# Kernel optimization log

Measured on AMD Instinct MI355X. Metric: run time of the kernel, lower is better.

## Reference

```python
import jax, jax.numpy as jnp
import numpy as np

DELTA_VAR = 0.5
DELTA_DIST = 1.5
ALPHA = 1.0
BETA = 1.0
C = 4096        # number of superpixels (static for segment_sum)
NE = 16384      # number of RAG edges


def setup_inputs() -> dict:
    key = jax.random.key(0)
    k1, k2, k3, k4 = jax.random.split(key, 4)
    embeddings = jax.random.normal(k1, (1, 16, 1024, 1024), dtype=jnp.float32)
    sp_seg = jax.random.randint(k2, (1, 1, 1024, 1024), 0, C)
    edges = jax.random.randint(k3, (2, NE), 0, C)
    weights = jax.random.uniform(k4, (NE,), dtype=jnp.float32)
    return {"embeddings": embeddings, "weights": weights, "sp_seg": sp_seg, "edges": edges}


def reference(embeddings, weights, sp_seg, edges):
    # embeddings: (1,E,H,W); sp_seg: (1,1,H,W) int labels in [0,C)
    E = embeddings.shape[1]
    emb = embeddings.reshape(E, -1).T          # (P,E) pixel-major
    seg = sp_seg.reshape(-1)                   # (P,)
    counts = jax.ops.segment_sum(jnp.ones(seg.shape, emb.dtype), seg, num_segments=C)  # (C,)
    sums = jax.ops.segment_sum(emb, seg, num_segments=C)                               # (C,E)
    n = jnp.maximum(counts, 1.0)               # guard empty segments (orig would div-by-0)
    means = sums / n[:, None]                  # (C,E) superpixel mean embeddings
    # intra-superpixel: d = 1 - <mean_c, emb_p> at pixels of segment c, hinge at delta_var,
    # normalized per-pixel by segment size, then averaged over C
    d_intra = 1.0 - jnp.sum(means[seg] * emb, axis=-1)            # (P,)
    intra = jnp.sum(jnp.maximum(d_intra - DELTA_VAR, 0.0) / n[seg]) / C
    # inter-superpixel: gather edge endpoint means, weighted hinge at delta_dist
    u, v = edges[0], edges[1]
    d_inter = 1.0 - jnp.sum(means[u] * means[v], axis=-1)         # (Ne,)
    inter = jnp.sum(jnp.maximum(DELTA_DIST - d_inter * weights, 0.0)) / edges.shape[1]
    return ALPHA * inter + BETA * intra
```

## Files before the change

kernel.cpp:

```cpp
#include <hip/hip_runtime.h>

#define C_SEG 4096
#define E_CH 16
#define NE_EDGES 16384
#define P_PIX (1024 * 1024)
#define NCHUNK 32
#define CHUNK_PIX (P_PIX / NCHUNK)
#define SCALE 262144.0f
#define INV_SCALE (1.0f / 262144.0f)


__global__ __launch_bounds__(512) void kA(const float* __restrict__ emb,
                                          const int* __restrict__ seg,
                                          float* __restrict__ sums_part,
                                          float* __restrict__ cnt_part) {
    __shared__ int bins[C_SEG];
    const int chunk = blockIdx.x;
    const int g = blockIdx.y;
    const int t = threadIdx.x;
    const int base = chunk * CHUNK_PIX;

    for (int i = t; i < C_SEG; i += 512) bins[i] = 0;
    __syncthreads();

    if (g == 16) {
        for (int it = 0; it < 16; ++it) {
            const int idx = base + (it * 512 + t) * 4;
            const int4 s4 = *(const int4*)(seg + idx);
            atomicAdd(&bins[s4.x], 1);
            atomicAdd(&bins[s4.y], 1);
            atomicAdd(&bins[s4.z], 1);
            atomicAdd(&bins[s4.w], 1);
        }
        __syncthreads();
        float* cd = cnt_part + (size_t)chunk * C_SEG;
        for (int i = t; i < C_SEG; i += 512) cd[i] = (float)bins[i];
    } else {
        const float* ec = emb + (size_t)g * P_PIX;
        for (int it = 0; it < 16; ++it) {
            const int idx = base + (it * 512 + t) * 4;
            const int4 s4 = *(const int4*)(seg + idx);
            const float4 v = *(const float4*)(ec + idx);
            atomicAdd(&bins[s4.x], __float2int_rn(v.x * SCALE));
            atomicAdd(&bins[s4.y], __float2int_rn(v.y * SCALE));
            atomicAdd(&bins[s4.z], __float2int_rn(v.z * SCALE));
            atomicAdd(&bins[s4.w], __float2int_rn(v.w * SCALE));
        }
        __syncthreads();
        float* dst = sums_part + ((size_t)g * NCHUNK + chunk) * C_SEG;
        for (int i = t; i < C_SEG; i += 512)
            dst[i] = (float)bins[i] * INV_SCALE;
    }
}

__global__ __launch_bounds__(256) void kB(const float* __restrict__ sums_part,
                                          const float* __restrict__ cnt_part,
                                          float* __restrict__ msum,
                                          float* __restrict__ inv_n) {
    const int vb = blockIdx.x, t = threadIdx.x;
    if (vb < 256) {
        const int c = vb >> 4;
        const int s = (vb & 15) * 256 + t;
        const float* src = sums_part + (size_t)c * NCHUNK * C_SEG + s;
        float acc = 0.0f;
#pragma unroll
        for (int k = 0; k < NCHUNK; ++k) acc += src[(size_t)k * C_SEG];
        msum[s * E_CH + c] = acc;
    } else {
        const int s = (vb - 256) * 256 + t;
        float acc = 0.0f;
#pragma unroll
        for (int k = 0; k < NCHUNK; ++k) acc += cnt_part[(size_t)k * C_SEG + s];
        inv_n[s] = 1.0f / fmaxf(acc, 1.0f);
    }
}

__global__ __launch_bounds__(256) void kC(const float* __restrict__ emb,
                                          const int* __restrict__ seg,
                                          const int* __restrict__ edges,
                                          const float* __restrict__ w,
                                          const float* __restrict__ msum,
                                          const float* __restrict__ inv_n,
                                          float* __restrict__ part) {
    const int b = blockIdx.x, t = threadIdx.x;
    const int q = b * 256 + t;
    const int4 s4 = *(const int4*)(seg + q * 4);

    float mA[16], mB[16], mC[16], mD[16];
#pragma unroll
    for (int j = 0; j < 4; ++j) {
        ((float4*)mA)[j] = ((const float4*)(msum + s4.x * E_CH))[j];
        ((float4*)mB)[j] = ((const float4*)(msum + s4.y * E_CH))[j];
        ((float4*)mC)[j] = ((const float4*)(msum + s4.z * E_CH))[j];
        ((float4*)mD)[j] = ((const float4*)(msum + s4.w * E_CH))[j];
    }
    const float inx = inv_n[s4.x], iny = inv_n[s4.y];
    const float inz = inv_n[s4.z], inw = inv_n[s4.w];

    const float4* emb4 = (const float4*)emb;
    float4 e[16];
#pragma unroll
    for (int c = 0; c < 16; ++c) e[c] = emb4[(size_t)c * (P_PIX / 4) + q];

    float dx = 0.f, dy = 0.f, dz = 0.f, dw = 0.f;
#pragma unroll
    for (int c = 0; c < 16; ++c) {
        dx = fmaf(e[c].x, mA[c], dx);
        dy = fmaf(e[c].y, mB[c], dy);
        dz = fmaf(e[c].z, mC[c], dz);
        dw = fmaf(e[c].w, mD[c], dw);
    }

    float v = (fmaxf(0.5f - inx * dx, 0.0f) * inx +
               fmaxf(0.5f - iny * dy, 0.0f) * iny +
               fmaxf(0.5f - inz * dz, 0.0f) * inz +
               fmaxf(0.5f - inw * dw, 0.0f) * inw) *
              (1.0f / (float)C_SEG);

    if (t < 16) {
        const int e2 = b * 16 + t;
        const int u = edges[e2];
        const int vv = edges[NE_EDGES + e2];
        const float4* mu = (const float4*)(msum + u * E_CH);
        const float4* mv = (const float4*)(msum + vv * E_CH);
        float dot = 0.0f;
#pragma unroll
        for (int j = 0; j < 4; ++j) {
            const float4 a = mu[j];
            const float4 bb = mv[j];
            dot = fmaf(a.x, bb.x, dot);
            dot = fmaf(a.y, bb.y, dot);
            dot = fmaf(a.z, bb.z, dot);
            dot = fmaf(a.w, bb.w, dot);
        }
        const float d = 1.0f - inv_n[u] * inv_n[vv] * dot;
        v += fmaxf(1.5f - d * w[e2], 0.0f) * (1.0f / (float)NE_EDGES);
    }

    for (int o = 32; o > 0; o >>= 1) v += __shfl_down(v, o, 64);
    __shared__ float red[4];
    if ((t & 63) == 0) red[t >> 6] = v;
    __syncthreads();
    if (t == 0) part[b] = red[0] + red[1] + red[2] + red[3];
}

__global__ __launch_bounds__(256) void kF(const float* __restrict__ part,
                                          float* __restrict__ out) {
    float v = 0.0f;
    for (int i = threadIdx.x; i < 1024; i += 256) v += part[i];
    for (int o = 32; o > 0; o >>= 1) v += __shfl_down(v, o, 64);
    __shared__ float red[4];
    const int t = threadIdx.x;
    if ((t & 63) == 0) red[t >> 6] = v;
    __syncthreads();
    if (t == 0) out[0] = red[0] + red[1] + red[2] + red[3];
}

extern "C" void kernel_launch(void* const* d_in, const int* in_sizes, int n_in,
                              void* d_out, int out_size, void* d_ws,
                              size_t ws_size, hipStream_t stream) {
    const float* emb = (const float*)d_in[0];
    const float* weights = (const float*)d_in[1];
    const int* seg = (const int*)d_in[2];
    const int* edges = (const int*)d_in[3];
    float* out = (float*)d_out;

    char* ws = (char*)d_ws;
    float* sums_part = (float*)(ws);
    float* cnt_part = (float*)(ws + 0x800000);
    float* msum = (float*)(ws + 0x880000);
    float* invn = (float*)(ws + 0x8C0000);
    float* part = (float*)(ws + 0x8C4000);

    dim3 gA(NCHUNK, 17);
    kA<<<gA, 512, 0, stream>>>(emb, seg, sums_part, cnt_part);
    kB<<<272, 256, 0, stream>>>(sums_part, cnt_part, msum, invn);
    kC<<<1024, 256, 0, stream>>>(emb, seg, edges, weights, msum, invn, part);
    kF<<<1, 256, 0, stream>>>(part, out);
}
```

Baseline: 134.5 us.

## Pack two channel sums into 64-bit shared atomics and store normalized means

The segment-sum kernel now packs two biased fixed-point channel values into a single 64-bit shared-memory atomic. This halves the number of atomic operations and the number of blocks that re-read the segment labels. The reduction kernel sums raw integers exactly, removes the bias, and writes normalized means, so the loss kernel no longer multiplies by the inverse count. The loss kernel also goes from four pixels per thread to two, with twice as many blocks, to cut register pressure. The bias makes 32-bit lane overflow possible if per-chunk sums grow large, and 64-bit LDS atomics may be slower per operation.

Measured after the change: 142.4 us. +5.9%, slower.

```diff
diff --git a/kernel.cpp b/kernel.cpp
--- a/kernel.cpp
+++ b/kernel.cpp
@@ -8,121 +8,134 @@
 #define CHUNK_PIX (P_PIX / NCHUNK)
 #define SCALE 262144.0f
 #define INV_SCALE (1.0f / 262144.0f)
+#define BIAS 4194304
 
 
 __global__ __launch_bounds__(512) void kA(const float* __restrict__ emb,
                                           const int* __restrict__ seg,
-                                          float* __restrict__ sums_part,
-                                          float* __restrict__ cnt_part) {
-    __shared__ int bins[C_SEG];
+                                          int* __restrict__ sums_raw,
+                                          int* __restrict__ cnt_raw) {
+    __shared__ unsigned long long bins[C_SEG];
     const int chunk = blockIdx.x;
     const int g = blockIdx.y;
     const int t = threadIdx.x;
     const int base = chunk * CHUNK_PIX;
 
-    for (int i = t; i < C_SEG; i += 512) bins[i] = 0;
-    __syncthreads();
-
-    if (g == 16) {
+    if (g == 8) {
+        int* ib = (int*)bins;
+        for (int i = t; i < C_SEG; i += 512) ib[i] = 0;
+        __syncthreads();
         for (int it = 0; it < 16; ++it) {
             const int idx = base + (it * 512 + t) * 4;
             const int4 s4 = *(const int4*)(seg + idx);
-            atomicAdd(&bins[s4.x], 1);
-            atomicAdd(&bins[s4.y], 1);
-            atomicAdd(&bins[s4.z], 1);
-            atomicAdd(&bins[s4.w], 1);
+            atomicAdd(&ib[s4.x], 1);
+            atomicAdd(&ib[s4.y], 1);
+            atomicAdd(&ib[s4.z], 1);
+            atomicAdd(&ib[s4.w], 1);
         }
         __syncthreads();
-        float* cd = cnt_part + (size_t)chunk * C_SEG;
-        for (int i = t; i < C_SEG; i += 512) cd[i] = (float)bins[i];
+        int* cd = cnt_raw + (size_t)chunk * C_SEG;
+        for (int i = t; i < C_SEG; i += 512) cd[i] = ib[i];
     } else {
-        const float* ec = emb + (size_t)g * P_PIX;
+        for (int i = t; i < C_SEG; i += 512) bins[i] = 0ull;
+        __syncthreads();
+        const float* ea = emb + (size_t)(2 * g) * P_PIX;
+        const float* eb = emb + (size_t)(2 * g + 1) * P_PIX;
         for (int it = 0; it < 16; ++it) {
             const int idx = base + (it * 512 + t) * 4;
             const int4 s4 = *(const int4*)(seg + idx);
-            const float4 v = *(const float4*)(ec + idx);
-            atomicAdd(&bins[s4.x], __float2int_rn(v.x * SCALE));
-            atomicAdd(&bins[s4.y], __float2int_rn(v.y * SCALE));
-            atomicAdd(&bins[s4.z], __float2int_rn(v.z * SCALE));
-            atomicAdd(&bins[s4.w], __float2int_rn(v.w * SCALE));
+            const float4 va = *(const float4*)(ea + idx);
+            const float4 vb = *(const float4*)(eb + idx);
+            const unsigned long long p0 =
+                ((unsigned long long)(unsigned)(__float2int_rn(vb.x * SCALE) + BIAS) << 32) |
+                (unsigned)(__float2int_rn(va.x * SCALE) + BIAS);
+            const unsigned long long p1 =
+                ((unsigned long long)(unsigned)(__float2int_rn(vb.y * SCALE) + BIAS) << 32) |
+                (unsigned)(__float2int_rn(va.y * SCALE) + BIAS);
+            const unsigned long long p2 =
+                ((unsigned long long)(unsigned)(__float2int_rn(vb.z * SCALE) + BIAS) << 32) |
+                (unsigned)(__float2int_rn(va.z * SCALE) + BIAS);
+            const unsigned long long p3 =
+                ((unsigned long long)(unsigned)(__float2int_rn(vb.w * SCALE) + BIAS) << 32) |
+                (unsigned)(__float2int_rn(va.w * SCALE) + BIAS);
+            atomicAdd(&bins[s4.x], p0);
+            atomicAdd(&bins[s4.y], p1);
+            atomicAdd(&bins[s4.z], p2);
+            atomicAdd(&bins[s4.w], p3);
         }
         __syncthreads();
-        float* dst = sums_part + ((size_t)g * NCHUNK + chunk) * C_SEG;
-        for (int i = t; i < C_SEG; i += 512)
-            dst[i] = (float)bins[i] * INV_SCALE;
+        int* da = sums_raw + ((size_t)(2 * g) * NCHUNK + chunk) * C_SEG;
+        int* db = sums_raw + ((size_t)(2 * g + 1) * NCHUNK + chunk) * C_SEG;
+        for (int i = t; i < C_SEG; i += 512) {
+            const unsigned long long v = bins[i];
+            da[i] = (int)(unsigned)(v & 0xffffffffull);
+            db[i] = (int)(unsigned)(v >> 32);
+        }
     }
 }
 
-__global__ __launch_bounds__(256) void kB(const float* __restrict__ sums_part,
-                                          const float* __restrict__ cnt_part,
-                                          float* __restrict__ msum,
+__global__ __launch_bounds__(256) void kB(const int* __restrict__ sums_raw,
+                                          const int* __restrict__ cnt_raw,
+                                          float* __restrict__ mean,
                                           float* __restrict__ inv_n) {
     const int vb = blockIdx.x, t = threadIdx.x;
-    if (vb < 256) {
-        const int c = vb >> 4;
-        const int s = (vb & 15) * 256 + t;
-        const float* src = sums_part + (size_t)c * NCHUNK * C_SEG + s;
-        float acc = 0.0f;
+    const int c = vb >> 4;
+    const int s = (vb & 15) * 256 + t;
+    const int* src = sums_raw + (size_t)c * NCHUNK * C_SEG + s;
+    long long acc = 0;
+    int cnt = 0;
 #pragma unroll
-        for (int k = 0; k < NCHUNK; ++k) acc += src[(size_t)k * C_SEG];
-        msum[s * E_CH + c] = acc;
-    } else {
-        const int s = (vb - 256) * 256 + t;
-        float acc = 0.0f;
-#pragma unroll
-        for (int k = 0; k < NCHUNK; ++k) acc += cnt_part[(size_t)k * C_SEG + s];
-        inv_n[s] = 1.0f / fmaxf(acc, 1.0f);
+    for (int k = 0; k < NCHUNK; ++k) {
+        acc += src[(size_t)k * C_SEG];
+        cnt += cnt_raw[(size_t)k * C_SEG + s];
     }
+    acc -= (long long)cnt * (long long)BIAS;
+    const float invn = 1.0f / fmaxf((float)cnt, 1.0f);
+    mean[s * E_CH + c] = (float)acc * INV_SCALE * invn;
+    if (c == 0) inv_n[s] = invn;
 }
 
 __global__ __launch_bounds__(256) void kC(const float* __restrict__ emb,
                                           const int* __restrict__ seg,
                                           const int* __restrict__ edges,
                                           const float* __restrict__ w,
-                                          const float* __restrict__ msum,
+                                          const float* __restrict__ mean,
                                           const float* __restrict__ inv_n,
                                           float* __restrict__ part) {
     const int b = blockIdx.x, t = threadIdx.x;
     const int q = b * 256 + t;
-    const int4 s4 = *(const int4*)(seg + q * 4);
+    const int2 s2 = *(const int2*)(seg + q * 2);
 
-    float mA[16], mB[16], mC[16], mD[16];
+    float mA[16], mB[16];
 #pragma unroll
     for (int j = 0; j < 4; ++j) {
-        ((float4*)mA)[j] = ((const float4*)(msum + s4.x * E_CH))[j];
-        ((float4*)mB)[j] = ((const float4*)(msum + s4.y * E_CH))[j];
-        ((float4*)mC)[j] = ((const float4*)(msum + s4.z * E_CH))[j];
-        ((float4*)mD)[j] = ((const float4*)(msum + s4.w * E_CH))[j];
+        ((float4*)mA)[j] = ((const float4*)(mean + s2.x * E_CH))[j];
+        ((float4*)mB)[j] = ((const float4*)(mean + s2.y * E_CH))[j];
     }
-    const float inx = inv_n[s4.x], iny = inv_n[s4.y];
-    const float inz = inv_n[s4.z], inw = inv_n[s4.w];
+    const float inx = inv_n[s2.x], iny = inv_n[s2.y];
 
-    const float4* emb4 = (const float4*)emb;
-    float4 e[16];
+    const float2* emb2 = (const float2*)emb;
+    float2 e[16];
 #pragma unroll
-    for (int c = 0; c < 16; ++c) e[c] = emb4[(size_t)c * (P_PIX / 4) + q];
+    for (int c = 0; c < 16; ++c) e[c] = emb2[(size_t)c * (P_PIX / 2) + q];
 
-    float dx = 0.f, dy = 0.f, dz = 0.f, dw = 0.f;
+    float dx = 0.f, dy = 0.f;
 #pragma unroll
     for (int c = 0; c < 16; ++c) {
         dx = fmaf(e[c].x, mA[c], dx);
         dy = fmaf(e[c].y, mB[c], dy);
-        dz = fmaf(e[c].z, mC[c], dz);
-        dw = fmaf(e[c].w, mD[c], dw);
     }
 
-    float v = (fmaxf(0.5f - inx * dx, 0.0f) * inx +
-               fmaxf(0.5f - iny * dy, 0.0f) * iny +
-               fmaxf(0.5f - inz * dz, 0.0f) * inz +
-               fmaxf(0.5f - inw * dw, 0.0f) * inw) *
+    float v = (fmaxf(0.5f - dx, 0.0f) * inx +
+               fmaxf(0.5f - dy, 0.0f) * iny) *
               (1.0f / (float)C_SEG);
 
-    if (t < 16) {
-        const int e2 = b * 16 + t;
+    if (t < 8) {
+        const int e2 = b * 8 + t;
         const int u = edges[e2];
         const int vv = edges[NE_EDGES + e2];
-        const float4* mu = (const float4*)(msum + u * E_CH);
-        const float4* mv = (const float4*)(msum + vv * E_CH);
+        const float4* mu = (const float4*)(mean + u * E_CH);
+        const float4* mv = (const float4*)(mean + vv * E_CH);
         float dot = 0.0f;
 #pragma unroll
         for (int j = 0; j < 4; ++j) {
@@ -133,7 +146,7 @@
             dot = fmaf(a.z, bb.z, dot);
             dot = fmaf(a.w, bb.w, dot);
         }
-        const float d = 1.0f - inv_n[u] * inv_n[vv] * dot;
+        const float d = 1.0f - dot;
         v += fmaxf(1.5f - d * w[e2], 0.0f) * (1.0f / (float)NE_EDGES);
     }
 
@@ -147,7 +160,7 @@
 __global__ __launch_bounds__(256) void kF(const float* __restrict__ part,
                                           float* __restrict__ out) {
     float v = 0.0f;
-    for (int i = threadIdx.x; i < 1024; i += 256) v += part[i];
+    for (int i = threadIdx.x; i < 2048; i += 256) v += part[i];
     for (int o = 32; o > 0; o >>= 1) v += __shfl_down(v, o, 64);
     __shared__ float red[4];
     const int t = threadIdx.x;
@@ -166,15 +179,15 @@
     float* out = (float*)d_out;
 
     char* ws = (char*)d_ws;
-    float* sums_part = (float*)(ws);
-    float* cnt_part = (float*)(ws + 0x800000);
-    float* msum = (float*)(ws + 0x880000);
+    int* sums_raw = (int*)(ws);
+    int* cnt_raw = (int*)(ws + 0x800000);
+    float* mean = (float*)(ws + 0x880000);
     float* invn = (float*)(ws + 0x8C0000);
     float* part = (float*)(ws + 0x8C4000);
 
-    dim3 gA(NCHUNK, 17);
-    kA<<<gA, 512, 0, stream>>>(emb, seg, sums_part, cnt_part);
-    kB<<<272, 256, 0, stream>>>(sums_part, cnt_part, msum, invn);
-    kC<<<1024, 256, 0, stream>>>(emb, seg, edges, weights, msum, invn, part);
+    dim3 gA(NCHUNK, 9);
+    kA<<<gA, 512, 0, stream>>>(emb, seg, sums_raw, cnt_raw);
+    kB<<<256, 256, 0, stream>>>(sums_raw, cnt_raw, mean, invn);
+    kC<<<2048, 256, 0, stream>>>(emb, seg, edges, weights, mean, invn, part);
     kF<<<1, 256, 0, stream>>>(part, out);
 }
```
